# Kernel tuning notes

Measured on AMD Instinct MI355X. Metric: run time of the kernel, lower is better.

Reference implementation:

```python
import jax, jax.numpy as jnp
import numpy as np

N = 50000
E = 1_600_000
IN_C = 128
HID = 64
HEADS = 2
OUT_C = 16
NEG_SLOPE = 0.2
EPS = 1e-16


def setup_inputs() -> dict:
    key = jax.random.key(0)
    ks = jax.random.split(key, 10)
    x = jax.random.normal(ks[0], (N, IN_C), dtype=jnp.float32)
    edge_index = jax.random.randint(ks[1], (2, E), 0, N, dtype=jnp.int64)
    # layer 1: in -> HEADS * HID, concat=True
    s1 = 1.0 / np.sqrt(IN_C)
    W1 = jax.random.normal(ks[2], (IN_C, HEADS * HID), dtype=jnp.float32) * s1
    att_src1 = jax.random.normal(ks[3], (HEADS, HID), dtype=jnp.float32) * (1.0 / np.sqrt(HID))
    att_dst1 = jax.random.normal(ks[4], (HEADS, HID), dtype=jnp.float32) * (1.0 / np.sqrt(HID))
    b1 = jnp.zeros((HEADS * HID,), dtype=jnp.float32)
    # layer 2: HEADS*HID -> OUT_C, heads=1
    s2 = 1.0 / np.sqrt(HEADS * HID)
    W2 = jax.random.normal(ks[5], (HEADS * HID, OUT_C), dtype=jnp.float32) * s2
    att_src2 = jax.random.normal(ks[6], (1, OUT_C), dtype=jnp.float32) * (1.0 / np.sqrt(OUT_C))
    att_dst2 = jax.random.normal(ks[7], (1, OUT_C), dtype=jnp.float32) * (1.0 / np.sqrt(OUT_C))
    b2 = jnp.zeros((OUT_C,), dtype=jnp.float32)
    return {"x": x, "W1": W1, "att_src1": att_src1, "att_dst1": att_dst1, "b1": b1,
            "W2": W2, "att_src2": att_src2, "att_dst2": att_dst2, "b2": b2,
            "edge_index": edge_index}


def gat_conv(x, edge_index, W, att_src, att_dst, bias, heads, out_ch):
    """PyG-style GATConv: per-head linear, additive attention, softmax over
    incoming edges of each destination node, scatter-add aggregation."""
    n = x.shape[0]
    src, dst = edge_index[0], edge_index[1]
    h = (x @ W).reshape(n, heads, out_ch)                # [N,H,C]
    a_src = jnp.einsum('nhc,hc->nh', h, att_src)          # [N,H]
    a_dst = jnp.einsum('nhc,hc->nh', h, att_dst)          # [N,H]
    e = a_src[src] + a_dst[dst]                           # [E,H]
    e = jnp.where(e >= 0, e, NEG_SLOPE * e)               # LeakyReLU(0.2)
    e_max = jax.ops.segment_max(e, dst, num_segments=n)   # [N,H]
    e_max = jax.lax.stop_gradient(jnp.where(jnp.isfinite(e_max), e_max, 0.0))
    e_exp = jnp.exp(e - e_max[dst])                       # [E,H]
    denom = jax.ops.segment_sum(e_exp, dst, num_segments=n)  # [N,H]
    alpha = e_exp / (denom[dst] + EPS)                    # [E,H]
    msg = h[src] * alpha[:, :, None]                      # [E,H,C] (dominant traffic)
    out = jax.ops.segment_sum(msg, dst, num_segments=n)   # [N,H,C]
    return out.reshape(n, heads * out_ch) + bias


def reference(x, W1, att_src1, att_dst1, b1, W2, att_src2, att_dst2, b2, edge_index):
    h = gat_conv(x, edge_index, W1, att_src1, att_dst1, b1, HEADS, HID)
    h = jax.nn.elu(h)
    h = gat_conv(h, edge_index, W2, att_src2, att_dst2, b2, 1, OUT_C)
    return jax.nn.softmax(h, axis=1)
```

## Files before the change

kernel.cpp:

```cpp
#include <hip/hip_runtime.h>
#include <hip/hip_fp16.h>
#include <cstdint>
#include <cstddef>

#define N_NODES 50000
#define N_EDGES 1600000
#define NEG_SLOPE 0.2f
#define GAT_EPS 1e-16f

#define NCHUNK 128
#define CE (N_EDGES / NCHUNK)
#define NBKT 196
#define GEMM_BLOCKS 782

typedef _Float16 half8v __attribute__((ext_vector_type(8)));
typedef _Float16 half4v __attribute__((ext_vector_type(4)));
typedef float f32x4 __attribute__((ext_vector_type(4)));



__global__ __launch_bounds__(256) void k_gh(
    const float* __restrict__ x, const float* __restrict__ W1,
    const float* __restrict__ W2, const float* __restrict__ b1,
    const float* __restrict__ att_src, const float* __restrict__ att_dst,
    _Float16* __restrict__ h1p, float* __restrict__ a_src, float* __restrict__ a_dst,
    const int* __restrict__ ei, int* __restrict__ coarse,
    float* __restrict__ w2tp, float* __restrict__ b1p) {
    __shared__ __align__(16) char smem[34816];
    int t = threadIdx.x;
    int b = blockIdx.x;
    if (b == GEMM_BLOCKS + NCHUNK) {
        for (int i = t; i < 2112; i += 256) {
            int j = i / 132, kp = i % 132;
            float v = 0.f;
            if (kp < 128) {
                int real = (kp & 7) * 16 + (kp >> 3);
                v = W2[real * 16 + j];
            }
            w2tp[i] = v;
        }
        if (t < 128) {
            int real = (t & 7) * 16 + (t >> 3);
            b1p[t] = b1[real];
        }
        return;
    }
    if (b >= GEMM_BLOCKS) {
        int* h = (int*)smem;
        int g = b - GEMM_BLOCKS;
        if (t < NBKT) h[t] = 0;
        __syncthreads();
        int e0 = g * CE;
        for (int e = e0 + t; e < e0 + CE; e += 256)
            atomicAdd(&h[ei[N_EDGES + e] >> 8], 1);
        __syncthreads();
        if (t < NBKT) coarse[t * NCHUNK + g] = h[t];
        return;
    }
    _Float16* wl = (_Float16*)smem;
    for (int j = t; j < 16384; j += 256) {
        int k = j >> 7, c = j & 127;
        wl[c * 136 + k] = (_Float16)W1[j];
    }
    __syncthreads();
    int wv = t >> 6, lane = t & 63;
    int m = lane & 15, q = lane >> 4;
    int nb = b * 64 + wv * 16;
    int grow = nb + m;
    const float* xrow = x + (size_t)((grow < N_NODES) ? grow : (N_NODES - 1)) * 128;
    f32x4 acc[8];
#pragma unroll
    for (int ct = 0; ct < 8; ++ct) acc[ct] = (f32x4){0.f, 0.f, 0.f, 0.f};
#pragma unroll
    for (int kc = 0; kc < 4; ++kc) {
        float4 u0 = *(const float4*)(xrow + kc * 32 + q * 8);
        float4 u1 = *(const float4*)(xrow + kc * 32 + q * 8 + 4);
        half8v a;
        a[0] = (_Float16)u0.x; a[1] = (_Float16)u0.y;
        a[2] = (_Float16)u0.z; a[3] = (_Float16)u0.w;
        a[4] = (_Float16)u1.x; a[5] = (_Float16)u1.y;
        a[6] = (_Float16)u1.z; a[7] = (_Float16)u1.w;
#pragma unroll
        for (int ct = 0; ct < 8; ++ct) {
            half8v bf = *(const half8v*)(wl + (ct * 16 + m) * 136 + kc * 32 + q * 8);
            acc[ct] = __builtin_amdgcn_mfma_f32_16x16x32_f16(a, bf, acc[ct], 0, 0, 0);
        }
    }
    float att_s[8], att_d[8];
#pragma unroll
    for (int ct = 0; ct < 8; ++ct) {
        att_s[ct] = att_src[ct * 16 + m];
        att_d[ct] = att_dst[ct * 16 + m];
    }
#pragma unroll
    for (int r = 0; r < 4; ++r) {
        int gn = nb + q * 4 + r;
        half8v hv;
        float ps0 = 0.f, ps1 = 0.f, pd0 = 0.f, pd1 = 0.f;
#pragma unroll
        for (int ct = 0; ct < 8; ++ct) {
            float v = acc[ct][r];
            hv[ct] = (_Float16)v;
            if (ct < 4) { ps0 += v * att_s[ct]; pd0 += v * att_d[ct]; }
            else        { ps1 += v * att_s[ct]; pd1 += v * att_d[ct]; }
        }
#pragma unroll
        for (int off = 8; off >= 1; off >>= 1) {
            ps0 += __shfl_xor(ps0, off, 64);
            ps1 += __shfl_xor(ps1, off, 64);
            pd0 += __shfl_xor(pd0, off, 64);
            pd1 += __shfl_xor(pd1, off, 64);
        }
        if (gn < N_NODES) {
            *(half8v*)(h1p + (size_t)gn * 128 + m * 8) = hv;
            if (m == 0) {
                a_src[gn * 2 + 0] = ps0;
                a_src[gn * 2 + 1] = ps1;
                a_dst[gn * 2 + 0] = pd0;
                a_dst[gn * 2 + 1] = pd1;
            }
        }
    }
}


__global__ __launch_bounds__(1024) void k_cscan(const int* __restrict__ coarse,
                                                int* __restrict__ cbase,
                                                int* __restrict__ bb,
                                                int* __restrict__ row_start) {
    __shared__ int cl[NBKT * NCHUNK];
    __shared__ int btot[NBKT];
    __shared__ int bbase[NBKT];
    int t = threadIdx.x;
    for (int i = t; i < NBKT * NCHUNK; i += 1024) cl[i] = coarse[i];
    __syncthreads();
    if (t < NBKT) {
        int s = 0;
        for (int g = 0; g < NCHUNK; ++g) s += cl[t * NCHUNK + g];
        btot[t] = s;
    }
    __syncthreads();
    if (t == 0) {
        int base = 0;
        for (int b = 0; b < NBKT; ++b) { bbase[b] = base; base += btot[b]; }
    }
    __syncthreads();
    if (t < NBKT) {
        int run = bbase[t];
        bb[t] = run;
        for (int g = 0; g < NCHUNK; ++g) {
            cbase[t * NCHUNK + g] = run;
            run += cl[t * NCHUNK + g];
        }
    }
    if (t == 0) { bb[NBKT] = N_EDGES; row_start[N_NODES] = N_EDGES; }
}

__global__ __launch_bounds__(256) void k_partition(const int* __restrict__ ei,
                                                   const int* __restrict__ cbase,
                                                   int2* __restrict__ part) {
    __shared__ int loc[NBKT];
    int t = threadIdx.x, g = blockIdx.x;
    if (t < NBKT) loc[t] = cbase[t * NCHUNK + g];
    __syncthreads();
    int e0 = g * CE;
    for (int e = e0 + t; e < e0 + CE; e += 256) {
        int s = ei[e], d = ei[N_EDGES + e];
        int slot = atomicAdd(&loc[d >> 8], 1);
        part[slot] = make_int2(s, d);
    }
}

__global__ __launch_bounds__(256) void k_local(const int2* __restrict__ part,
                                               const int* __restrict__ bb,
                                               const float* __restrict__ a_src1,
                                               const float* __restrict__ a_dst1,
                                               int* __restrict__ row_start,
                                               int4* __restrict__ csr) {
    __shared__ int hist[256];
    __shared__ int fillv[256];
    __shared__ float2 adl[256];
    __shared__ int wtot[4];
    int t = threadIdx.x, b = blockIdx.x;
    int n0 = b << 8;
    int es = bb[b], ee = bb[b + 1];
    hist[t] = 0;
    if (n0 + t < N_NODES) adl[t] = ((const float2*)a_dst1)[n0 + t];
    __syncthreads();
    for (int e = es + t; e < ee; e += 256) atomicAdd(&hist[part[e].y - n0], 1);
    __syncthreads();
    int lane = t & 63, w = t >> 6;
    int v = hist[t], x = v;
#pragma unroll
    for (int off = 1; off < 64; off <<= 1) {
        int y = __shfl_up(x, off, 64);
        if (lane >= off) x += y;
    }
    if (lane == 63) wtot[w] = x;
    __syncthreads();
    int woff = 0;
    for (int i = 0; i < w; ++i) woff += wtot[i];
    int excl = woff + x - v;
    if (n0 + t < N_NODES) row_start[n0 + t] = es + excl;
    fillv[t] = excl;
    __syncthreads();
    for (int e = es + t; e < ee; e += 256) {
        int2 sd = part[e];
        int j = sd.y - n0;
        int slot = es + atomicAdd(&fillv[j], 1);
        float2 as = ((const float2*)a_src1)[sd.x];
        float2 ad = adl[j];
        float e0 = as.x + ad.x; e0 = (e0 >= 0.f) ? e0 : NEG_SLOPE * e0;
        float e1 = as.y + ad.y; e1 = (e1 >= 0.f) ? e1 : NEG_SLOPE * e1;
        csr[slot] = make_int4(sd.x, __float_as_int(expf(e0)), __float_as_int(expf(e1)), 0);
    }
}


__global__ __launch_bounds__(256) void k_agg1f(
    const int* __restrict__ row_start, const int4* __restrict__ csr,
    const _Float16* __restrict__ h1p, const float* __restrict__ b1p,
    const float* __restrict__ w2tp,
    const float* __restrict__ att_src2, const float* __restrict__ att_dst2,
    float* __restrict__ h2, float* __restrict__ as2, float* __restrict__ ad2) {
    __shared__ float w2l[16 * 132];
    __shared__ float rows[4][128];
    int t = threadIdx.x;
    for (int i = t; i < 528; i += 256) ((float4*)w2l)[i] = ((const float4*)w2tp)[i];
    __syncthreads();
    int wv = t >> 6, lane = t & 63;
    int d = blockIdx.x * 4 + wv;
    int row = row_start[d], end = row_start[d + 1];
    int half = lane >> 5;
    int L = lane & 31;
    int c0 = L * 4;
    int head = L & 1;
    float den = 0.f;
    float4 acc = make_float4(0.f, 0.f, 0.f, 0.f);
    int i = row;
    for (; i + 8 <= end; i += 8) {
#pragma unroll
        for (int p = 0; p < 4; ++p) {
            int idx = i + 2 * p + half;
            int4 e4 = csr[idx];
            float we = head ? __int_as_float(e4.z) : __int_as_float(e4.y);
            half4v hv = *(const half4v*)(h1p + (size_t)e4.x * 128 + c0);
            den += we;
            acc.x += we * (float)hv[0];
            acc.y += we * (float)hv[1];
            acc.z += we * (float)hv[2];
            acc.w += we * (float)hv[3];
        }
    }
    for (; i < end; i += 2) {
        int idx = i + half;
        bool ok = idx < end;
        int idxc = ok ? idx : i;
        int4 e4 = csr[idxc];
        float we = head ? __int_as_float(e4.z) : __int_as_float(e4.y);
        if (!ok) we = 0.f;
        half4v hv = *(const half4v*)(h1p + (size_t)e4.x * 128 + c0);
        den += we;
        acc.x += we * (float)hv[0];
        acc.y += we * (float)hv[1];
        acc.z += we * (float)hv[2];
        acc.w += we * (float)hv[3];
    }
    den += __shfl_xor(den, 32, 64);
    acc.x += __shfl_xor(acc.x, 32, 64);
    acc.y += __shfl_xor(acc.y, 32, 64);
    acc.z += __shfl_xor(acc.z, 32, 64);
    acc.w += __shfl_xor(acc.w, 32, 64);
    float inv = 1.f / (den + GAT_EPS);
    float4 bv = ((const float4*)b1p)[L];
    float o0 = acc.x * inv + bv.x;
    float o1 = acc.y * inv + bv.y;
    float o2 = acc.z * inv + bv.z;
    float o3 = acc.w * inv + bv.w;
    o0 = (o0 > 0.f) ? o0 : expm1f(o0);
    o1 = (o1 > 0.f) ? o1 : expm1f(o1);
    o2 = (o2 > 0.f) ? o2 : expm1f(o2);
    o3 = (o3 > 0.f) ? o3 : expm1f(o3);
    if (half == 0) *(float4*)(&rows[wv][c0]) = make_float4(o0, o1, o2, o3);
    int j = lane & 15, q = lane >> 4;
    const float* r = rows[wv];
    const float* wt = &w2l[j * 132];
    int k0 = q * 32;
    float acc2 = 0.f;
#pragma unroll
    for (int sI = 0; sI < 8; ++sI) {
        int sp = ((sI + q) & 7) * 4;
        float4 rv = *(const float4*)(r + k0 + sp);
        float4 w4 = *(const float4*)(wt + k0 + sp);
        acc2 += rv.x * w4.x + rv.y * w4.y + rv.z * w4.z + rv.w * w4.w;
    }
    acc2 += __shfl_xor(acc2, 16, 64);
    acc2 += __shfl_xor(acc2, 32, 64);
    if (lane < 16) {
        h2[(size_t)d * 16 + j] = acc2;
        float ps = acc2 * att_src2[j];
        float pd = acc2 * att_dst2[j];
#pragma unroll
        for (int off = 8; off >= 1; off >>= 1) {
            ps += __shfl_xor(ps, off, 64);
            pd += __shfl_xor(pd, off, 64);
        }
        if (lane == 0) { as2[d] = ps; ad2[d] = pd; }
    }
}


__global__ __launch_bounds__(256) void k_agg2(
    const int* __restrict__ row_start, const int4* __restrict__ csr,
    const float* __restrict__ h2, const float* __restrict__ as2,
    const float* __restrict__ ad2, const float* __restrict__ b2,
    float* __restrict__ out) {
    int t = threadIdx.x;
    int wv = t >> 6, lane = t & 63;
    int d = blockIdx.x * 4 + wv;
    int row = row_start[d], end = row_start[d + 1];
    float ad = ad2[d];
    int c = lane & 15, q = lane >> 4;
    float den = 0.f, acc = 0.f;
    for (int base = row; base < end; base += 64) {
        int idx = base + lane;
        float w = 0.f; int s = 0;
        if (idx < end) {
            s = csr[idx].x;
            float e = as2[s] + ad;
            e = (e >= 0.f) ? e : NEG_SLOPE * e;
            w = expf(e);
        }
        den += w;
        int m = end - base; if (m > 64) m = 64;
        int jj = 0;
        for (; jj + 8 <= m; jj += 8) {
            float w0 = __shfl(w, jj + q, 64);
            int   s0 = __shfl(s, jj + q, 64);
            float w1_ = __shfl(w, jj + 4 + q, 64);
            int   s1 = __shfl(s, jj + 4 + q, 64);
            float h0 = h2[(size_t)s0 * 16 + c];
            float h1_ = h2[(size_t)s1 * 16 + c];
            acc += w0 * h0 + w1_ * h1_;
        }
        for (; jj < m; jj += 4) {
            float wj = __shfl(w, jj + q, 64);
            int sj = __shfl(s, jj + q, 64);
            acc += wj * h2[(size_t)sj * 16 + c];
        }
    }
#pragma unroll
    for (int off = 32; off >= 1; off >>= 1) den += __shfl_xor(den, off, 64);
    acc += __shfl_xor(acc, 16, 64);
    acc += __shfl_xor(acc, 32, 64);
    float v = acc / (den + GAT_EPS) + b2[c];
    float mmax = v;
#pragma unroll
    for (int off = 8; off >= 1; off >>= 1) mmax = fmaxf(mmax, __shfl_xor(mmax, off, 16));
    float ex = expf(v - mmax);
    float sum = ex;
#pragma unroll
    for (int off = 8; off >= 1; off >>= 1) sum += __shfl_xor(sum, off, 16);
    if (lane < 16) out[(size_t)d * 16 + c] = ex / sum;
}


extern "C" void kernel_launch(void* const* d_in, const int* in_sizes, int n_in,
                              void* d_out, int out_size, void* d_ws, size_t ws_size,
                              hipStream_t stream) {
    const float* x        = (const float*)d_in[0];
    const float* W1       = (const float*)d_in[1];
    const float* att_src1 = (const float*)d_in[2];
    const float* att_dst1 = (const float*)d_in[3];
    const float* b1       = (const float*)d_in[4];
    const float* W2       = (const float*)d_in[5];
    const float* att_src2 = (const float*)d_in[6];
    const float* att_dst2 = (const float*)d_in[7];
    const float* b2       = (const float*)d_in[8];
    const int*   ei       = (const int*)d_in[9];

    char* p = (char*)d_ws;
    auto alloc = [&](size_t bytes) {
        char* r = p;
        p += (bytes + 255) & ~(size_t)255;
        return r;
    };
    _Float16* h1p  = (_Float16*)alloc(sizeof(_Float16) * (size_t)N_NODES * 128);
    float* w2tp    = (float*)alloc(sizeof(float) * 16 * 132);
    float* b1p     = (float*)alloc(sizeof(float) * 128);
    float* h2      = (float*)alloc(sizeof(float) * (size_t)N_NODES * 16);
    float* a_src   = (float*)alloc(sizeof(float) * N_NODES * 2);
    float* a_dst   = (float*)alloc(sizeof(float) * N_NODES * 2);
    float* as2     = (float*)alloc(sizeof(float) * N_NODES);
    float* ad2     = (float*)alloc(sizeof(float) * N_NODES);
    int* coarse    = (int*)alloc(sizeof(int) * NBKT * NCHUNK);
    int* cbase     = (int*)alloc(sizeof(int) * NBKT * NCHUNK);
    int* bb        = (int*)alloc(sizeof(int) * (NBKT + 1));
    int* row_start = (int*)alloc(sizeof(int) * (N_NODES + 1));
    int2* part     = (int2*)alloc(sizeof(int2) * (size_t)N_EDGES);
    int4* csr      = (int4*)alloc(sizeof(int4) * (size_t)N_EDGES);

    k_gh<<<GEMM_BLOCKS + NCHUNK + 1, 256, 0, stream>>>(x, W1, W2, b1, att_src1, att_dst1,
                                                       h1p, a_src, a_dst, ei, coarse, w2tp, b1p);
    k_cscan<<<1, 1024, 0, stream>>>(coarse, cbase, bb, row_start);
    k_partition<<<NCHUNK, 256, 0, stream>>>(ei, cbase, part);
    k_local<<<NBKT, 256, 0, stream>>>(part, bb, a_src, a_dst, row_start, csr);
    k_agg1f<<<N_NODES / 4, 256, 0, stream>>>(row_start, csr, h1p, b1p, w2tp, att_src2, att_dst2, h2, as2, ad2);
    k_agg2<<<N_NODES / 4, 256, 0, stream>>>(row_start, csr, h2, as2, ad2, b2, (float*)d_out);
}
```

Measured before the change: 265.2 us.

## Restructure layer-1 aggregation: stage edges in LDS, 16-byte gathers per lane

Layer-1 aggregation now has each wave load 64 CSR edge records at once into shared memory. Four groups of 16 lanes then each process one edge at a time, and each lane gathers 8 fp16 values (16 bytes) that mix both heads. The old layout used 2 edges per iteration with 8-byte gathers and a separate global CSR read per lane per edge. The change widens memory transactions, cuts redundant CSR loads, and gives more edges in flight per wave. In exchange it needs more accumulator registers, extra LDS, and a four-way cross-lane reduction at the end. Separately, the layer-2 aggregation inner loop gets an unroll-by-2 pragma.

Result: no change. 262.2 us (-1.1%).

```diff
diff --git a/kernel.cpp b/kernel.cpp
--- a/kernel.cpp
+++ b/kernel.cpp
@@ -225,63 +225,81 @@
     float* __restrict__ h2, float* __restrict__ as2, float* __restrict__ ad2) {
     __shared__ float w2l[16 * 132];
     __shared__ float rows[4][128];
+    __shared__ int4 elds[4][64];
     int t = threadIdx.x;
     for (int i = t; i < 528; i += 256) ((float4*)w2l)[i] = ((const float4*)w2tp)[i];
     __syncthreads();
     int wv = t >> 6, lane = t & 63;
     int d = blockIdx.x * 4 + wv;
     int row = row_start[d], end = row_start[d + 1];
-    int half = lane >> 5;
-    int L = lane & 31;
-    int c0 = L * 4;
-    int head = L & 1;
-    float den = 0.f;
-    float4 acc = make_float4(0.f, 0.f, 0.f, 0.f);
-    int i = row;
-    for (; i + 8 <= end; i += 8) {
-#pragma unroll
-        for (int p = 0; p < 4; ++p) {
-            int idx = i + 2 * p + half;
-            int4 e4 = csr[idx];
-            float we = head ? __int_as_float(e4.z) : __int_as_float(e4.y);
-            half4v hv = *(const half4v*)(h1p + (size_t)e4.x * 128 + c0);
-            den += we;
-            acc.x += we * (float)hv[0];
-            acc.y += we * (float)hv[1];
-            acc.z += we * (float)hv[2];
-            acc.w += we * (float)hv[3];
-        }
-    }
-    for (; i < end; i += 2) {
-        int idx = i + half;
-        bool ok = idx < end;
-        int idxc = ok ? idx : i;
+    int m16 = lane & 15;
+    int qt = lane >> 4;
+    uint32_t moff = (uint32_t)m16 * 16u;
+    const char* hbase = (const char*)h1p;
+    float den0 = 0.f, den1 = 0.f;
+    float acc[8];
+#pragma unroll
+    for (int i = 0; i < 8; ++i) acc[i] = 0.f;
+    for (int base = row; base < end; base += 64) {
+        int m = end - base;
+        if (m > 64) m = 64;
+        int idx = base + lane;
+        int idxc = (idx < end) ? idx : (end - 1);
         int4 e4 = csr[idxc];
-        float we = head ? __int_as_float(e4.z) : __int_as_float(e4.y);
-        if (!ok) we = 0.f;
-        half4v hv = *(const half4v*)(h1p + (size_t)e4.x * 128 + c0);
-        den += we;
-        acc.x += we * (float)hv[0];
-        acc.y += we * (float)hv[1];
-        acc.z += we * (float)hv[2];
-        acc.w += we * (float)hv[3];
-    }
-    den += __shfl_xor(den, 32, 64);
-    acc.x += __shfl_xor(acc.x, 32, 64);
-    acc.y += __shfl_xor(acc.y, 32, 64);
-    acc.z += __shfl_xor(acc.z, 32, 64);
-    acc.w += __shfl_xor(acc.w, 32, 64);
-    float inv = 1.f / (den + GAT_EPS);
-    float4 bv = ((const float4*)b1p)[L];
-    float o0 = acc.x * inv + bv.x;
-    float o1 = acc.y * inv + bv.y;
-    float o2 = acc.z * inv + bv.z;
-    float o3 = acc.w * inv + bv.w;
-    o0 = (o0 > 0.f) ? o0 : expm1f(o0);
-    o1 = (o1 > 0.f) ? o1 : expm1f(o1);
-    o2 = (o2 > 0.f) ? o2 : expm1f(o2);
-    o3 = (o3 > 0.f) ? o3 : expm1f(o3);
-    if (half == 0) *(float4*)(&rows[wv][c0]) = make_float4(o0, o1, o2, o3);
+        if (idx >= end) { e4.y = 0; e4.z = 0; }
+        elds[wv][lane] = e4;
+        int nc = (m + 3) >> 2;
+        auto step = [&](int p) {
+            int4 md = elds[wv][p * 4 + qt];
+            float w0 = __int_as_float(md.y);
+            float w1 = __int_as_float(md.z);
+            uint32_t off = ((uint32_t)md.x << 8) + moff;
+            half8v hv = *(const half8v*)(hbase + off);
+            den0 += w0;
+            den1 += w1;
+            acc[0] += w0 * (float)hv[0];
+            acc[1] += w0 * (float)hv[1];
+            acc[2] += w0 * (float)hv[2];
+            acc[3] += w0 * (float)hv[3];
+            acc[4] += w1 * (float)hv[4];
+            acc[5] += w1 * (float)hv[5];
+            acc[6] += w1 * (float)hv[6];
+            acc[7] += w1 * (float)hv[7];
+        };
+        int p = 0;
+        for (; p + 4 <= nc; p += 4) {
+            step(p); step(p + 1); step(p + 2); step(p + 3);
+        }
+        for (; p < nc; ++p) step(p);
+    }
+#pragma unroll
+    for (int i = 0; i < 8; ++i) {
+        acc[i] += __shfl_xor(acc[i], 16, 64);
+        acc[i] += __shfl_xor(acc[i], 32, 64);
+    }
+    den0 += __shfl_xor(den0, 16, 64);
+    den0 += __shfl_xor(den0, 32, 64);
+    den1 += __shfl_xor(den1, 16, 64);
+    den1 += __shfl_xor(den1, 32, 64);
+    float inv0 = 1.f / (den0 + GAT_EPS);
+    float inv1 = 1.f / (den1 + GAT_EPS);
+    float4 blo = ((const float4*)b1p)[m16 * 2];
+    float4 bhi = ((const float4*)b1p)[m16 * 2 + 1];
+    float o[8];
+    o[0] = acc[0] * inv0 + blo.x;
+    o[1] = acc[1] * inv0 + blo.y;
+    o[2] = acc[2] * inv0 + blo.z;
+    o[3] = acc[3] * inv0 + blo.w;
+    o[4] = acc[4] * inv1 + bhi.x;
+    o[5] = acc[5] * inv1 + bhi.y;
+    o[6] = acc[6] * inv1 + bhi.z;
+    o[7] = acc[7] * inv1 + bhi.w;
+#pragma unroll
+    for (int i = 0; i < 8; ++i) o[i] = (o[i] > 0.f) ? o[i] : expm1f(o[i]);
+    if (qt == 0) {
+        *(float4*)(&rows[wv][m16 * 8]) = make_float4(o[0], o[1], o[2], o[3]);
+        *(float4*)(&rows[wv][m16 * 8 + 4]) = make_float4(o[4], o[5], o[6], o[7]);
+    }
     int j = lane & 15, q = lane >> 4;
     const float* r = rows[wv];
     const float* wt = &w2l[j * 132];
@@ -334,6 +352,7 @@
         den += w;
         int m = end - base; if (m > 64) m = 64;
         int jj = 0;
+#pragma unroll 2
         for (; jj + 8 <= m; jj += 8) {
             float w0 = __shfl(w, jj + q, 64);
             int   s0 = __shfl(s, jj + q, 64);
```
